# Kernel optimization log

Hardware: AMD Instinct MI355X
Metric: run time of the kernel (lower is better)

Reference implementation:

```python
import jax, jax.numpy as jnp
import numpy as np

H, DH = 16, 64          # num_heads, dim_head
DIM = 1024              # dim_ltn
EPS = 1e-5


def setup_inputs() -> dict:
    key = jax.random.key(0)
    ks = jax.random.split(key, 8)
    b, n_txt, t, m = 2, 2048, 4, 256
    text = jax.random.normal(ks[0], (b, n_txt, DIM), dtype=jnp.float32)
    image = jax.random.normal(ks[1], (b, t, m, DIM), dtype=jnp.float32)
    locations = jax.random.randint(ks[2], (b, n_txt), 0, 2)  # 0/1 media markers
    s = DIM ** -0.5
    Wq = jax.random.normal(ks[3], (DIM, H * DH), dtype=jnp.float32) * s
    Wkv = jax.random.normal(ks[4], (DIM, 2 * H * DH), dtype=jnp.float32) * s
    Wo = jax.random.normal(ks[5], (H * DH, DIM), dtype=jnp.float32) * s
    ln_gamma = jnp.ones((DIM,), dtype=jnp.float32)
    ln_beta = jnp.zeros((DIM,), dtype=jnp.float32)
    return {"text": text, "image": image, "locations": locations,
            "Wq": Wq, "Wkv": Wkv, "Wo": Wo,
            "ln_gamma": ln_gamma, "ln_beta": ln_beta}


def reference(text, image, locations, Wq, Wkv, Wo, ln_gamma, ln_beta):
    scale = DH ** -0.5
    b, t, m, d = image.shape
    # LayerNorm(text)
    mu = text.mean(-1, keepdims=True)
    var = ((text - mu) ** 2).mean(-1, keepdims=True)
    tn = (text - mu) / jnp.sqrt(var + EPS) * ln_gamma + ln_beta
    img = image.reshape(b, t * m, d)             # b (t m) d
    q = tn @ Wq                                  # b n (h dh)
    k, v = jnp.split(img @ Wkv, 2, axis=-1)      # each b tm (h dh)
    split_heads = lambda x: x.reshape(x.shape[0], x.shape[1], H, DH).transpose(0, 2, 1, 3)
    q, k, v = split_heads(q), split_heads(k), split_heads(v)
    attn = jnp.einsum('bhid,bhjd->bhij', q, k) * scale   # b h n (t m)
    txt_time = jnp.cumsum(locations, axis=-1)            # b n : media index per text token
    viz_time = jnp.repeat(jnp.arange(1, t + 1), m)       # (t m)
    # only_attend_to_immediate -> equality mask
    mask = txt_time[:, None, :, None] == viz_time[None, None, None, :]
    neg = -jnp.finfo(attn.dtype).max
    attn = jnp.where(mask, attn, neg)
    attn = jax.nn.softmax(attn, axis=-1)
    # zero attention for text tokens before any media (txt_time == 0)
    attn = jnp.where((txt_time == 0)[:, None, :, None], 0.0, attn)
    out = jnp.einsum('bhij,bhjd->bhid', attn, v)
    out = out.transpose(0, 2, 1, 3).reshape(b, -1, H * DH)
    return out @ Wo
```

## Files before the change

### kernel.cpp

```cpp
#include <hip/hip_runtime.h>

#define BATCH 2
#define NTXT  2048
#define TMED  4
#define MMED  256
#define TM    (TMED * MMED)
#define DIM   1024
#define NH    16
#define DHD   64
#define KVW   2048
#define RMAX  256
#define RT    32

typedef _Float16 f16x8 __attribute__((ext_vector_type(8)));
typedef float    f32x4 __attribute__((ext_vector_type(4)));

__global__ __launch_bounds__(1024) void k1_scan_cvt_tr(
    const int* __restrict__ loc, const float* __restrict__ image,
    const float* __restrict__ Wkv, int* __restrict__ tt, int* __restrict__ seg,
    float* __restrict__ ipart, _Float16* __restrict__ img16,
    _Float16* __restrict__ WkvT, float* __restrict__ zbase) {
  __shared__ float tile[64][65];
  __shared__ int wtot[16];
  __shared__ int wmin[2][16];
  const int idx = blockIdx.x;
  const int tid = threadIdx.x;
  if (idx < BATCH) {
    const int b = idx;
    const int lane = tid & 63, w = tid >> 6;
    const int e0 = tid * 2;
    const int a0 = loc[b * NTXT + e0], a1 = loc[b * NTXT + e0 + 1];
    const int p = a0 + a1;
    int incl = p;
#pragma unroll
    for (int off = 1; off < 64; off <<= 1) {
      const int t2 = __shfl_up(incl, off, 64);
      if (lane >= off) incl += t2;
    }
    if (lane == 63) wtot[w] = incl;
    __syncthreads();
    if (tid < 16) {
      const int v = wtot[tid];
      int inc2 = v;
#pragma unroll
      for (int off = 1; off < 16; off <<= 1) {
        const int t3 = __shfl_up(inc2, off, 64);
        if (tid >= off) inc2 += t3;
      }
      wtot[tid] = inc2 - v;
    }
    __syncthreads();
    const int base = wtot[w] + (incl - p);
    const int t0v = base + a0, t1v = t0v + a1;
    tt[b * NTXT + e0]     = t0v;
    tt[b * NTXT + e0 + 1] = t1v;
    {
      const int c1 = (t1v >= 1) ? ((t0v >= 1) ? e0 : e0 + 1) : NTXT;
      const int c5 = (t1v >= 5) ? ((t0v >= 5) ? e0 : e0 + 1) : NTXT;
      const unsigned long long b1 = __ballot(t1v >= 1);
      const unsigned long long b5 = __ballot(t1v >= 5);
      int m1 = NTXT, m5 = NTXT;
      if (b1) m1 = __shfl(c1, __ffsll(b1) - 1, 64);
      if (b5) m5 = __shfl(c5, __ffsll(b5) - 1, 64);
      if (lane == 0) { wmin[0][w] = m1; wmin[1][w] = m5; }
    }
    __syncthreads();
    if (tid == 0) {
      int s = NTXT, e = NTXT;
#pragma unroll
      for (int i = 0; i < 16; i++) {
        s = min(s, wmin[0][i]);
        e = min(e, wmin[1][i]);
      }
      seg[b * 2]     = s;
      seg[b * 2 + 1] = e - s;
    }
  } else if (idx < BATCH + 256) {
    const int j = idx - BATCH;
    const int b = j >> 7, rt = j & 127;
    const size_t base = (size_t)(b * TM + rt * 8) * DIM + tid;
    const float* p = image + base;
    _Float16* q = img16 + base;
    float s = 0.f;
#pragma unroll
    for (int r = 0; r < 8; r++) {
      const float v = p[(size_t)r * DIM];
      s += v;
      q[(size_t)r * DIM] = (_Float16)v;
    }
    ipart[(size_t)(b * 128 + rt) * DIM + tid] = s;
  } else if (idx < BATCH + 256 + 512) {
    const int j2 = idx - BATCH - 256;
    const int k0 = (j2 & 15) * 64, n0 = (j2 >> 4) * 64;
    const int r = tid >> 4, c4 = (tid & 15) * 4;
    const float4 v = *reinterpret_cast<const float4*>(
        Wkv + (size_t)(k0 + r) * KVW + n0 + c4);
    tile[r][c4 + 0] = v.x; tile[r][c4 + 1] = v.y;
    tile[r][c4 + 2] = v.z; tile[r][c4 + 3] = v.w;
    __syncthreads();
    if (tid < 512) {
      const int n = tid >> 3, kc = (tid & 7) * 8;
      f16x8 h;
#pragma unroll
      for (int u = 0; u < 8; u++) h[u] = (_Float16)tile[kc + u][n];
      *reinterpret_cast<f16x8*>(WkvT + (size_t)(n0 + n) * DIM + k0 + kc) = h;
    }
  } else {
    const int j = idx - (BATCH + 256 + 512);
    float4* z = reinterpret_cast<float4*>(zbase);
    const float4 zv = {0.f, 0.f, 0.f, 0.f};
    for (int i = j * 1024 + tid; i < 132096; i += 16 * 1024) z[i] = zv;
  }
}

__global__ __launch_bounds__(256) void k2_prep(
    const float* __restrict__ Wkv, const float* __restrict__ text,
    const float* __restrict__ gamma, const float* __restrict__ beta,
    const int* __restrict__ seg, const float* __restrict__ ipart,
    float* __restrict__ tn, float* __restrict__ vbar,
    float* __restrict__ out) {
  __shared__ float red[256];
  const int idx = blockIdx.x;
  const int tid = threadIdx.x;
  if (idx < 64) {
    const int b = idx >> 5, rt = idx & 31;
    const int i0 = seg[b * 2];
    const int cnt = min(seg[b * 2 + 1], RMAX);
    for (int r = rt; r < cnt; r += RT) {
      const float* xrow = text + (size_t)(b * NTXT + i0 + r) * DIM;
      float x[4];
      float s = 0.f;
#pragma unroll
      for (int u = 0; u < 4; u++) { x[u] = xrow[tid + 256 * u]; s += x[u]; }
      red[tid] = s; __syncthreads();
      for (int st = 128; st > 0; st >>= 1) {
        if (tid < st) red[tid] += red[tid + st];
        __syncthreads();
      }
      const float mu = red[0] * (1.0f / DIM); __syncthreads();
      float vs = 0.f;
#pragma unroll
      for (int u = 0; u < 4; u++) { float d = x[u] - mu; vs += d * d; }
      red[tid] = vs; __syncthreads();
      for (int st = 128; st > 0; st >>= 1) {
        if (tid < st) red[tid] += red[tid + st];
        __syncthreads();
      }
      const float rstd = rsqrtf(red[0] * (1.0f / DIM) + 1e-5f); __syncthreads();
      float* trow = tn + (size_t)(b * RMAX + r) * DIM;
#pragma unroll
      for (int u = 0; u < 4; u++) {
        const int c = tid + 256 * u;
        trow[c] = (x[u] - mu) * rstd * gamma[c] + beta[c];
      }
      __syncthreads();
    }
  } else if (idx < 128) {
    const int j = idx - 64;
    const int b = j >> 5, et = (j >> 3) & 3, cc = j & 7;
    const int e = et * 256 + tid;
    const int c0 = cc * 128;
    if (tid < 128) {
      float s = 0.f;
      for (int p = 0; p < 128; p++)
        s += ipart[(size_t)(b * 128 + p) * DIM + c0 + tid];
      red[tid] = s * (1.0f / (float)TM);
    }
    __syncthreads();
    float s = 0.f;
    for (int c = 0; c < 128; c++)
      s += red[c] * Wkv[(size_t)(c0 + c) * KVW + DIM + e];
    atomicAdd(&vbar[b * DIM + e], s);
  } else {
    const int b = idx - 128;
    const int i0 = seg[b * 2];
    const int cnt = min(seg[b * 2 + 1], RMAX);
    for (int r = 0; r < cnt; r++) {
      float* orow = out + (size_t)(b * NTXT + i0 + r) * DIM;
      for (int c = tid; c < DIM; c += 256) orow[c] = 0.f;
    }
  }
}

__global__ __launch_bounds__(512) void k3_gemm_qproj_obar(
    const _Float16* __restrict__ img16, const _Float16* __restrict__ WkvT,
    const float* __restrict__ Wq, const float* __restrict__ Wo,
    const float* __restrict__ tn, const float* __restrict__ vbar,
    const int* __restrict__ seg, _Float16* __restrict__ kv16,
    float* __restrict__ qbuf, float* __restrict__ obar) {
  __shared__ __align__(16) char smem[32768];
  const int idx = blockIdx.x;
  const int tid = threadIdx.x;
  if (idx < 256) {
    _Float16* As = (_Float16*)smem;
    _Float16* Bs = As + 128 * 64;
    const int lane = tid & 63, wid = tid >> 6;
    const int wm = wid & 3, wn = wid >> 2;
    const int row0 = (idx >> 4) * 128, col0 = (idx & 15) * 128;
    const int srow = tid >> 3, skc = (tid & 7) * 8;
    const int frow = lane & 15, fq = lane >> 4;
    const int swk = skc ^ ((srow & 7) << 3);
    f32x4 acc[2][4] = {};
    f16x8 a0v = *reinterpret_cast<const f16x8*>(
        img16 + (size_t)(row0 + srow) * DIM + skc);
    f16x8 a1v = *reinterpret_cast<const f16x8*>(
        img16 + (size_t)(row0 + srow + 64) * DIM + skc);
    f16x8 b0v = *reinterpret_cast<const f16x8*>(
        WkvT + (size_t)(col0 + srow) * DIM + skc);
    f16x8 b1v = *reinterpret_cast<const f16x8*>(
        WkvT + (size_t)(col0 + srow + 64) * DIM + skc);
    for (int k0 = 0; k0 < DIM; k0 += 64) {
      __syncthreads();
      *reinterpret_cast<f16x8*>(As + srow * 64 + swk)        = a0v;
      *reinterpret_cast<f16x8*>(As + (srow + 64) * 64 + swk) = a1v;
      *reinterpret_cast<f16x8*>(Bs + srow * 64 + swk)        = b0v;
      *reinterpret_cast<f16x8*>(Bs + (srow + 64) * 64 + swk) = b1v;
      __syncthreads();
      if (k0 + 64 < DIM) {
        a0v = *reinterpret_cast<const f16x8*>(
            img16 + (size_t)(row0 + srow) * DIM + k0 + 64 + skc);
        a1v = *reinterpret_cast<const f16x8*>(
            img16 + (size_t)(row0 + srow + 64) * DIM + k0 + 64 + skc);
        b0v = *reinterpret_cast<const f16x8*>(
            WkvT + (size_t)(col0 + srow) * DIM + k0 + 64 + skc);
        b1v = *reinterpret_cast<const f16x8*>(
            WkvT + (size_t)(col0 + srow + 64) * DIM + k0 + 64 + skc);
      }
      f16x8 af[2][2], bf[2][4];
#pragma unroll
      for (int kk = 0; kk < 2; kk++) {
#pragma unroll
        for (int mt = 0; mt < 2; mt++) {
          const int r = wm * 32 + mt * 16 + frow;
          af[kk][mt] = *reinterpret_cast<const f16x8*>(
              As + r * 64 + ((kk * 32 + fq * 8) ^ ((r & 7) << 3)));
        }
#pragma unroll
        for (int nt = 0; nt < 4; nt++) {
          const int c = wn * 64 + nt * 16 + frow;
          bf[kk][nt] = *reinterpret_cast<const f16x8*>(
              Bs + c * 64 + ((kk * 32 + fq * 8) ^ ((c & 7) << 3)));
        }
      }
#pragma unroll
      for (int kk = 0; kk < 2; kk++)
#pragma unroll
        for (int mt = 0; mt < 2; mt++)
#pragma unroll
          for (int nt = 0; nt < 4; nt++)
            acc[mt][nt] = __builtin_amdgcn_mfma_f32_16x16x32_f16(
                af[kk][mt], bf[kk][nt], acc[mt][nt], 0, 0, 0);
    }
#pragma unroll
    for (int mt = 0; mt < 2; mt++)
#pragma unroll
      for (int nt = 0; nt < 4; nt++) {
        const int col = col0 + wn * 64 + nt * 16 + frow;
#pragma unroll
        for (int r = 0; r < 4; r++) {
          const int row = row0 + wm * 32 + mt * 16 + fq * 4 + r;
          kv16[(size_t)row * KVW + col] = (_Float16)acc[mt][nt][r];
        }
      }
  } else if (idx < 320) {
    float* tn_s = (float*)smem;
    const int j = idx - 256;
    const int b = j >> 5, nt = (j >> 2) & 7, cc = j & 3;
    const int n0 = nt * 128, c0 = cc * 256;
    const int n = tid & 127, cs = tid >> 7;
    const int cnt = min(seg[b * 2 + 1], RMAX);
    for (int r0 = 0; r0 < cnt; r0 += 8) {
      const int rows = min(8, cnt - r0);
      for (int i = tid; i < 8 * 256; i += 512) {
        const int r = i >> 8, c = i & 255;
        tn_s[i] = (r < rows) ? tn[(size_t)(b * RMAX + r0 + r) * DIM + c0 + c]
                             : 0.f;
      }
      __syncthreads();
      float acc[8] = {};
      for (int ci = 0; ci < 64; ci++) {
        const int c = cs * 64 + ci;
        const float w = Wq[(size_t)(c0 + c) * DIM + n0 + n];
#pragma unroll
        for (int rr = 0; rr < 8; rr++) acc[rr] += tn_s[rr * 256 + c] * w;
      }
      for (int rr = 0; rr < rows; rr++)
        atomicAdd(&qbuf[(size_t)(b * RMAX + r0 + rr) * DIM + n0 + n], acc[rr]);
      __syncthreads();
    }
  } else {
    float* vb_s = (float*)smem;
    const int j = idx - 320;
    const int b = j >> 4, et = (j >> 3) & 1, cc = j & 7;
    const int e = et * 512 + tid;
    const int c0 = cc * 128;
    if (tid < 128) vb_s[tid] = vbar[b * DIM + c0 + tid];
    __syncthreads();
    float s = 0.f;
    for (int c = 0; c < 128; c++)
      s += vb_s[c] * Wo[(size_t)(c0 + c) * DIM + e];
    atomicAdd(&obar[b * DIM + e], s);
  }
}

__global__ __launch_bounds__(256) void k4_fill_attn(
    const float* __restrict__ text, const _Float16* __restrict__ kv16,
    const float* __restrict__ Wq, const float* __restrict__ Wo,
    const float* __restrict__ gamma, const float* __restrict__ beta,
    const int* __restrict__ tt, const int* __restrict__ seg,
    const float* __restrict__ obar, const float* __restrict__ qbuf,
    float* __restrict__ out) {
  __shared__ float red[256];
  __shared__ float pbuf[256];
  const int idx = blockIdx.x;
  const int tid = threadIdx.x;
  if (idx < BATCH * NTXT) {
    const int b = idx >> 11;
    const int i = idx & (NTXT - 1);
    const int t = tt[b * NTXT + i];
    float* orow = out + (size_t)(b * NTXT + i) * DIM;
    if (t == 0) {
      for (int c = tid; c < DIM; c += 256) orow[c] = 0.f;
      return;
    }
    if (t > TMED) {
      const float* ob = obar + b * DIM;
      for (int c = tid; c < DIM; c += 256) orow[c] = ob[c];
      return;
    }
    if (i - seg[b * 2] < RMAX) return;
    __shared__ float tns[DIM];
    __shared__ float qrow[DIM];
    __shared__ float oaccs[DIM];
    const float* xrow = text + (size_t)(b * NTXT + i) * DIM;
    float x[4];
    float s = 0.f;
#pragma unroll
    for (int u = 0; u < 4; u++) { x[u] = xrow[tid + 256 * u]; s += x[u]; }
    red[tid] = s; __syncthreads();
    for (int st = 128; st > 0; st >>= 1) {
      if (tid < st) red[tid] += red[tid + st];
      __syncthreads();
    }
    const float mu = red[0] * (1.0f / DIM); __syncthreads();
    float vs = 0.f;
#pragma unroll
    for (int u = 0; u < 4; u++) { float d = x[u] - mu; vs += d * d; }
    red[tid] = vs; __syncthreads();
    for (int st = 128; st > 0; st >>= 1) {
      if (tid < st) red[tid] += red[tid + st];
      __syncthreads();
    }
    const float rstd = rsqrtf(red[0] * (1.0f / DIM) + 1e-5f); __syncthreads();
#pragma unroll
    for (int u = 0; u < 4; u++) {
      const int c = tid + 256 * u;
      tns[c] = (x[u] - mu) * rstd * gamma[c] + beta[c];
    }
    __syncthreads();
    {
      float qa[4] = {0.f, 0.f, 0.f, 0.f};
      for (int c = 0; c < DIM; c++) {
        const float tv = tns[c];
        const float* w = Wq + (size_t)c * DIM + tid;
#pragma unroll
        for (int u = 0; u < 4; u++) qa[u] += tv * w[256 * u];
      }
#pragma unroll
      for (int u = 0; u < 4; u++) qrow[tid + 256 * u] = qa[u];
    }
    __syncthreads();
    const size_t kvrow0 = (size_t)(b * TM + (t - 1) * MMED) * KVW;
    const int d0 = tid & 63, g = tid >> 6;
    for (int h = 0; h < NH; h++) {
      const _Float16* krow = kv16 + kvrow0 + (size_t)tid * KVW + h * DHD;
      float sc = 0.f;
#pragma unroll
      for (int d = 0; d < DHD; d++) sc += qrow[h * DHD + d] * (float)krow[d];
      sc *= 0.125f;
      red[tid] = sc; __syncthreads();
      for (int st = 128; st > 0; st >>= 1) {
        if (tid < st) red[tid] = fmaxf(red[tid], red[tid + st]);
        __syncthreads();
      }
      const float mx = red[0]; __syncthreads();
      const float e = __expf(sc - mx);
      red[tid] = e; __syncthreads();
      for (int st = 128; st > 0; st >>= 1) {
        if (tid < st) red[tid] += red[tid + st];
        __syncthreads();
      }
      const float inv = 1.0f / red[0]; __syncthreads();
      pbuf[tid] = e * inv; __syncthreads();
      const _Float16* vbase = kv16 + kvrow0 + (size_t)(g * 64) * KVW + DIM + h * DHD + d0;
      float a = 0.f;
#pragma unroll 8
      for (int jj = 0; jj < 64; jj++) a += pbuf[g * 64 + jj] * (float)vbase[(size_t)jj * KVW];
      red[tid] = a; __syncthreads();
      if (tid < 64)
        oaccs[h * DHD + tid] = red[tid] + red[64 + tid] + red[128 + tid] + red[192 + tid];
      __syncthreads();
    }
    float oa[4] = {0.f, 0.f, 0.f, 0.f};
    for (int c = 0; c < DIM; c++) {
      const float ov = oaccs[c];
      const float* w = Wo + (size_t)c * DIM + tid;
#pragma unroll
      for (int u = 0; u < 4; u++) oa[u] += ov * w[256 * u];
    }
#pragma unroll
    for (int u = 0; u < 4; u++) orow[tid + 256 * u] = oa[u];
  } else {
    __shared__ float qs[DHD];
    __shared__ float osl[DHD];
    const int j = idx - BATCH * NTXT;
    const int h = j & 15, rt = (j >> 4) & 31, b = j >> 9;
    const int i0 = seg[b * 2];
    const int cnt = min(seg[b * 2 + 1], RMAX);
    const int d0 = tid & 63, g = tid >> 6;
    for (int r = rt; r < cnt; r += RT) {
      const int i = i0 + r;
      const int t = tt[b * NTXT + i];
      if (tid < 64) qs[tid] = qbuf[(size_t)(b * RMAX + r) * DIM + h * DHD + tid];
      __syncthreads();
      const size_t kvrow0 = (size_t)(b * TM + (t - 1) * MMED) * KVW;
      const _Float16* krow = kv16 + kvrow0 + (size_t)tid * KVW + h * DHD;
      float sc = 0.f;
#pragma unroll
      for (int d = 0; d < DHD; d += 8) {
        const f16x8 kk = *reinterpret_cast<const f16x8*>(krow + d);
#pragma unroll
        for (int u = 0; u < 8; u++) sc += qs[d + u] * (float)kk[u];
      }
      sc *= 0.125f;
      red[tid] = sc; __syncthreads();
      for (int st = 128; st > 0; st >>= 1) {
        if (tid < st) red[tid] = fmaxf(red[tid], red[tid + st]);
        __syncthreads();
      }
      const float mx = red[0]; __syncthreads();
      const float e = __expf(sc - mx);
      red[tid] = e; __syncthreads();
      for (int st = 128; st > 0; st >>= 1) {
        if (tid < st) red[tid] += red[tid + st];
        __syncthreads();
      }
      const float inv = 1.0f / red[0]; __syncthreads();
      pbuf[tid] = e * inv; __syncthreads();
      const _Float16* vbase = kv16 + kvrow0 + (size_t)(g * 64) * KVW + DIM + h * DHD + d0;
      float a = 0.f;
#pragma unroll 8
      for (int jj = 0; jj < 64; jj++) a += pbuf[g * 64 + jj] * (float)vbase[(size_t)jj * KVW];
      red[tid] = a; __syncthreads();
      if (tid < 64)
        osl[tid] = red[tid] + red[64 + tid] + red[128 + tid] + red[192 + tid];
      __syncthreads();
      float* orow = out + (size_t)(b * NTXT + i) * DIM;
#pragma unroll
      for (int u = 0; u < 4; u++) {
        const int c = tid + 256 * u;
        const float* w = Wo + (size_t)(h * DHD) * DIM + c;
        float s2 = 0.f;
#pragma unroll 8
        for (int d = 0; d < DHD; d++) s2 += osl[d] * w[(size_t)d * DIM];
        atomicAdd(&orow[c], s2);
      }
      __syncthreads();
    }
  }
}

extern "C" void kernel_launch(void* const* d_in, const int* in_sizes, int n_in,
                              void* d_out, int out_size, void* d_ws, size_t ws_size,
                              hipStream_t stream) {
  const float* text  = (const float*)d_in[0];
  const float* image = (const float*)d_in[1];
  const int*   loc   = (const int*)d_in[2];
  const float* Wq    = (const float*)d_in[3];
  const float* Wkv   = (const float*)d_in[4];
  const float* Wo    = (const float*)d_in[5];
  const float* gamma = (const float*)d_in[6];
  const float* beta  = (const float*)d_in[7];
  float* out = (float*)d_out;

  _Float16* kv16  = (_Float16*)d_ws;
  _Float16* WkvT  = kv16 + (size_t)BATCH * TM * KVW;
  _Float16* img16 = WkvT + (size_t)KVW * DIM;
  float*    tn    = (float*)(img16 + (size_t)BATCH * TM * DIM);
  float*    qbuf  = tn + (size_t)BATCH * RMAX * DIM;
  float*    vbar  = qbuf + (size_t)BATCH * RMAX * DIM;
  float*    obar  = vbar + BATCH * DIM;
  int*      tt    = (int*)(obar + BATCH * DIM);
  int*      seg   = tt + BATCH * NTXT;
  float*    ipart = (float*)(seg + 8);

  k1_scan_cvt_tr<<<BATCH + 256 + 512 + 16, 1024, 0, stream>>>(
      loc, image, Wkv, tt, seg, ipart, img16, WkvT, qbuf);
  k2_prep<<<130, 256, 0, stream>>>(Wkv, text, gamma, beta, seg, ipart,
                                   tn, vbar, out);
  k3_gemm_qproj_obar<<<352, 512, 0, stream>>>(img16, WkvT, Wq, Wo, tn, vbar,
                                              seg, kv16, qbuf, obar);
  k4_fill_attn<<<BATCH * NTXT + NH * RT * BATCH, 256, 0, stream>>>(
      text, kv16, Wq, Wo, gamma, beta, tt, seg, obar, qbuf, out);
}
```

Before: 152.8 us.

## Restructure attention by folding Wk into queries and Wv after probabilities

Replaces the full K/V projection GEMM over all image tokens with an algebraic reordering. Queries are multiplied by the per-head Wk slice to give U, scores are taken directly against fp16 image rows, and probabilities are multiplied by the transposed image before Wv and Wo are applied. This removes the large image×Wkv GEMM and the Wkv transpose. In exchange it adds six kernels with extra intermediate buffers (S, P16, pbar) and per-row scalar projection loops. Work now scales with the number of active rows times heads, so the cost depends on the media-marker layout.

```diff
diff --git a/kernel.cpp b/kernel.cpp
--- a/kernel.cpp
+++ b/kernel.cpp
@@ -10,463 +10,429 @@
 #define DHD   64
 #define KVW   2048
 #define RMAX  256
-#define RT    32
+#define MCAP  (RMAX * NH)
 
 typedef _Float16 f16x8 __attribute__((ext_vector_type(8)));
 typedef float    f32x4 __attribute__((ext_vector_type(4)));
 
-__global__ __launch_bounds__(1024) void k1_scan_cvt_tr(
+__device__ __forceinline__ void find5(const int* __restrict__ loc, int b,
+                                      int* posS, int tid) {
+  if (tid < 64) {
+    int pos[5] = {NTXT, NTXT, NTXT, NTXT, NTXT};
+    int found = 0;
+    for (int base = 0; base < NTXT && found < 5; base += 64) {
+      unsigned long long m = __ballot(loc[b * NTXT + base + tid] != 0);
+      while (m && found < 5) {
+        const int p = __ffsll(m) - 1;
+        pos[found++] = base + p;
+        m &= m - 1;
+      }
+    }
+    if (tid == 0) {
+#pragma unroll
+      for (int k = 0; k < 5; k++) posS[k] = pos[k];
+    }
+  }
+  __syncthreads();
+}
+
+__global__ __launch_bounds__(1024) void kA(
     const int* __restrict__ loc, const float* __restrict__ image,
-    const float* __restrict__ Wkv, int* __restrict__ tt, int* __restrict__ seg,
+    const float* __restrict__ text, const float* __restrict__ gamma,
+    const float* __restrict__ beta, int* __restrict__ seg,
     float* __restrict__ ipart, _Float16* __restrict__ img16,
-    _Float16* __restrict__ WkvT, float* __restrict__ zbase) {
-  __shared__ float tile[64][65];
-  __shared__ int wtot[16];
-  __shared__ int wmin[2][16];
+    _Float16* __restrict__ imgT16, float* __restrict__ tn,
+    float* __restrict__ out) {
+  __shared__ _Float16 cvt[32 * 1024];
+  __shared__ int posS[5];
+  __shared__ float wred[20];
   const int idx = blockIdx.x;
   const int tid = threadIdx.x;
   if (idx < BATCH) {
     const int b = idx;
-    const int lane = tid & 63, w = tid >> 6;
-    const int e0 = tid * 2;
-    const int a0 = loc[b * NTXT + e0], a1 = loc[b * NTXT + e0 + 1];
-    const int p = a0 + a1;
-    int incl = p;
-#pragma unroll
-    for (int off = 1; off < 64; off <<= 1) {
-      const int t2 = __shfl_up(incl, off, 64);
-      if (lane >= off) incl += t2;
-    }
-    if (lane == 63) wtot[w] = incl;
-    __syncthreads();
-    if (tid < 16) {
-      const int v = wtot[tid];
-      int inc2 = v;
-#pragma unroll
-      for (int off = 1; off < 16; off <<= 1) {
-        const int t3 = __shfl_up(inc2, off, 64);
-        if (tid >= off) inc2 += t3;
-      }
-      wtot[tid] = inc2 - v;
-    }
-    __syncthreads();
-    const int base = wtot[w] + (incl - p);
-    const int t0v = base + a0, t1v = t0v + a1;
-    tt[b * NTXT + e0]     = t0v;
-    tt[b * NTXT + e0 + 1] = t1v;
-    {
-      const int c1 = (t1v >= 1) ? ((t0v >= 1) ? e0 : e0 + 1) : NTXT;
-      const int c5 = (t1v >= 5) ? ((t0v >= 5) ? e0 : e0 + 1) : NTXT;
-      const unsigned long long b1 = __ballot(t1v >= 1);
-      const unsigned long long b5 = __ballot(t1v >= 5);
-      int m1 = NTXT, m5 = NTXT;
-      if (b1) m1 = __shfl(c1, __ffsll(b1) - 1, 64);
-      if (b5) m5 = __shfl(c5, __ffsll(b5) - 1, 64);
-      if (lane == 0) { wmin[0][w] = m1; wmin[1][w] = m5; }
-    }
-    __syncthreads();
+    find5(loc, b, posS, tid);
     if (tid == 0) {
-      int s = NTXT, e = NTXT;
-#pragma unroll
-      for (int i = 0; i < 16; i++) {
-        s = min(s, wmin[0][i]);
-        e = min(e, wmin[1][i]);
-      }
-      seg[b * 2]     = s;
-      seg[b * 2 + 1] = e - s;
-    }
-  } else if (idx < BATCH + 256) {
+#pragma unroll
+      for (int k = 0; k < 5; k++) seg[b * 8 + k] = posS[k];
+      int cnt = posS[4] - posS[0];
+      if (posS[0] >= NTXT) cnt = 0;
+      seg[b * 8 + 5] = min(cnt, RMAX);
+    }
+  } else if (idx < BATCH + 64) {
     const int j = idx - BATCH;
-    const int b = j >> 7, rt = j & 127;
-    const size_t base = (size_t)(b * TM + rt * 8) * DIM + tid;
-    const float* p = image + base;
-    _Float16* q = img16 + base;
+    const int b = j >> 5, jt = j & 31;
+    const int j0 = jt * 32;
+    const size_t rbase = (size_t)(b * TM + j0) * DIM + tid;
     float s = 0.f;
-#pragma unroll
-    for (int r = 0; r < 8; r++) {
-      const float v = p[(size_t)r * DIM];
+#pragma unroll 4
+    for (int r = 0; r < 32; r++) {
+      const float v = image[rbase + (size_t)r * DIM];
       s += v;
-      q[(size_t)r * DIM] = (_Float16)v;
-    }
-    ipart[(size_t)(b * 128 + rt) * DIM + tid] = s;
-  } else if (idx < BATCH + 256 + 512) {
-    const int j2 = idx - BATCH - 256;
-    const int k0 = (j2 & 15) * 64, n0 = (j2 >> 4) * 64;
-    const int r = tid >> 4, c4 = (tid & 15) * 4;
-    const float4 v = *reinterpret_cast<const float4*>(
-        Wkv + (size_t)(k0 + r) * KVW + n0 + c4);
-    tile[r][c4 + 0] = v.x; tile[r][c4 + 1] = v.y;
-    tile[r][c4 + 2] = v.z; tile[r][c4 + 3] = v.w;
-    __syncthreads();
-    if (tid < 512) {
-      const int n = tid >> 3, kc = (tid & 7) * 8;
-      f16x8 h;
-#pragma unroll
-      for (int u = 0; u < 8; u++) h[u] = (_Float16)tile[kc + u][n];
-      *reinterpret_cast<f16x8*>(WkvT + (size_t)(n0 + n) * DIM + k0 + kc) = h;
-    }
+      const _Float16 hv = (_Float16)v;
+      img16[rbase + (size_t)r * DIM] = hv;
+      cvt[r * 1024 + tid] = hv;
+    }
+    ipart[(b * 32 + jt) * 1024 + tid] = s;
+    __syncthreads();
+    f16x8 tv[4];
+#pragma unroll
+    for (int g = 0; g < 4; g++)
+#pragma unroll
+      for (int u = 0; u < 8; u++)
+        tv[g][u] = cvt[(g * 8 + u) * 1024 + tid];
+    _Float16* dst = imgT16 + (size_t)(b * DIM + tid) * TM + j0;
+#pragma unroll
+    for (int g = 0; g < 4; g++)
+      *reinterpret_cast<f16x8*>(dst + g * 8) = tv[g];
   } else {
-    const int j = idx - (BATCH + 256 + 512);
-    float4* z = reinterpret_cast<float4*>(zbase);
-    const float4 zv = {0.f, 0.f, 0.f, 0.f};
-    for (int i = j * 1024 + tid; i < 132096; i += 16 * 1024) z[i] = zv;
-  }
-}
-
-__global__ __launch_bounds__(256) void k2_prep(
-    const float* __restrict__ Wkv, const float* __restrict__ text,
-    const float* __restrict__ gamma, const float* __restrict__ beta,
-    const int* __restrict__ seg, const float* __restrict__ ipart,
-    float* __restrict__ tn, float* __restrict__ vbar,
-    float* __restrict__ out) {
-  __shared__ float red[256];
-  const int idx = blockIdx.x;
-  const int tid = threadIdx.x;
-  if (idx < 64) {
-    const int b = idx >> 5, rt = idx & 31;
-    const int i0 = seg[b * 2];
-    const int cnt = min(seg[b * 2 + 1], RMAX);
-    for (int r = rt; r < cnt; r += RT) {
-      const float* xrow = text + (size_t)(b * NTXT + i0 + r) * DIM;
-      float x[4];
-      float s = 0.f;
-#pragma unroll
-      for (int u = 0; u < 4; u++) { x[u] = xrow[tid + 256 * u]; s += x[u]; }
-      red[tid] = s; __syncthreads();
-      for (int st = 128; st > 0; st >>= 1) {
-        if (tid < st) red[tid] += red[tid + st];
+    const int b = idx - (BATCH + 64);
+    find5(loc, b, posS, tid);
+    const int pos0 = posS[0];
+    int cnt = posS[4] - pos0;
+    if (pos0 >= NTXT) cnt = 0;
+    cnt = min(cnt, RMAX);
+    for (int r = 0; r < cnt; r++) {
+      const float x = text[(size_t)(b * NTXT + pos0 + r) * DIM + tid];
+      float v = x;
+#pragma unroll
+      for (int off = 32; off; off >>= 1) v += __shfl_xor(v, off, 64);
+      if ((tid & 63) == 0) wred[tid >> 6] = v;
+      __syncthreads();
+      if (tid == 0) {
+        float t2 = 0.f;
+#pragma unroll
+        for (int q = 0; q < 16; q++) t2 += wred[q];
+        wred[16] = t2;
+      }
+      __syncthreads();
+      const float mu = wred[16] * (1.0f / DIM);
+      __syncthreads();
+      const float d = x - mu;
+      float v2 = d * d;
+#pragma unroll
+      for (int off = 32; off; off >>= 1) v2 += __shfl_xor(v2, off, 64);
+      if ((tid & 63) == 0) wred[tid >> 6] = v2;
+      __syncthreads();
+      if (tid == 0) {
+        float t2 = 0.f;
+#pragma unroll
+        for (int q = 0; q < 16; q++) t2 += wred[q];
+        wred[16] = t2;
+      }
+      __syncthreads();
+      const float rstd = rsqrtf(wred[16] * (1.0f / DIM) + 1e-5f);
+      __syncthreads();
+      tn[(size_t)(b * RMAX + r) * DIM + tid] = d * rstd * gamma[tid] + beta[tid];
+      out[(size_t)(b * NTXT + pos0 + r) * DIM + tid] = 0.f;
+    }
+  }
+}
+
+__global__ __launch_bounds__(256) void kB(
+    const float* __restrict__ Wq, const float* __restrict__ Wkv,
+    const float* __restrict__ tn, const int* __restrict__ seg,
+    const float* __restrict__ ipart, _Float16* __restrict__ U16,
+    float* __restrict__ vbar) {
+  __shared__ float tn_s[8 * 1024];
+  __shared__ float qred[4 * 8 * 64];
+  __shared__ float Qs[8 * 64];
+  __shared__ float wk_s[64 * 65];
+  __shared__ float ib_s[1024];
+  __shared__ float vred2[256];
+  const int idx = blockIdx.x;
+  const int tid = threadIdx.x;
+  if (idx < 32) {
+    const int b = idx >> 4, h = idx & 15;
+    const int cnt = seg[b * 8 + 5];
+    for (int ic0 = 0; ic0 < cnt; ic0 += 8) {
+      const int ni = min(8, cnt - ic0);
+      for (int k = tid; k < 8 * 1024; k += 256) {
+        const int r = k >> 10;
+        tn_s[k] = (r < ni) ? tn[(size_t)(b * RMAX + ic0 + r) * DIM + (k & 1023)]
+                           : 0.f;
+      }
+      __syncthreads();
+      {
+        const int d = tid & 63, cg = tid >> 6;
+        float qp[8] = {};
+        for (int c = cg * 256; c < cg * 256 + 256; c++) {
+          const float w = Wq[(size_t)c * DIM + h * DHD + d];
+#pragma unroll
+          for (int i2 = 0; i2 < 8; i2++) qp[i2] += tn_s[i2 * 1024 + c] * w;
+        }
+#pragma unroll
+        for (int i2 = 0; i2 < 8; i2++) qred[(cg * 8 + i2) * 64 + d] = qp[i2];
+      }
+      __syncthreads();
+      for (int k = tid; k < 512; k += 256) {
+        const int i2 = k >> 6, d = k & 63;
+        Qs[k] = qred[(0 * 8 + i2) * 64 + d] + qred[(1 * 8 + i2) * 64 + d] +
+                qred[(2 * 8 + i2) * 64 + d] + qred[(3 * 8 + i2) * 64 + d];
+      }
+      __syncthreads();
+      for (int cc = 0; cc < 16; cc++) {
+        for (int k = tid; k < 64 * 64; k += 256) {
+          const int row = k >> 6, col = k & 63;
+          wk_s[row * 65 + col] = Wkv[(size_t)(cc * 64 + row) * KVW + h * DHD + col];
+        }
         __syncthreads();
-      }
-      const float mu = red[0] * (1.0f / DIM); __syncthreads();
-      float vs = 0.f;
-#pragma unroll
-      for (int u = 0; u < 4; u++) { float d = x[u] - mu; vs += d * d; }
-      red[tid] = vs; __syncthreads();
-      for (int st = 128; st > 0; st >>= 1) {
-        if (tid < st) red[tid] += red[tid + st];
+        const int cl = tid & 63, ig = tid >> 6;
+#pragma unroll
+        for (int ii = 0; ii < 2; ii++) {
+          const int i2 = ig * 2 + ii;
+          if (i2 < ni) {
+            float u = 0.f;
+#pragma unroll 8
+            for (int d2 = 0; d2 < 64; d2++)
+              u += Qs[i2 * 64 + d2] * wk_s[cl * 65 + d2];
+            U16[((size_t)b * MCAP + (size_t)(ic0 + i2) * NH + h) * DIM +
+                cc * 64 + cl] = (_Float16)u;
+          }
+        }
         __syncthreads();
       }
-      const float rstd = rsqrtf(red[0] * (1.0f / DIM) + 1e-5f); __syncthreads();
-      float* trow = tn + (size_t)(b * RMAX + r) * DIM;
-#pragma unroll
-      for (int u = 0; u < 4; u++) {
-        const int c = tid + 256 * u;
-        trow[c] = (x[u] - mu) * rstd * gamma[c] + beta[c];
-      }
-      __syncthreads();
-    }
-  } else if (idx < 128) {
-    const int j = idx - 64;
-    const int b = j >> 5, et = (j >> 3) & 3, cc = j & 7;
-    const int e = et * 256 + tid;
-    const int c0 = cc * 128;
-    if (tid < 128) {
-      float s = 0.f;
-      for (int p = 0; p < 128; p++)
-        s += ipart[(size_t)(b * 128 + p) * DIM + c0 + tid];
-      red[tid] = s * (1.0f / (float)TM);
-    }
-    __syncthreads();
-    float s = 0.f;
-    for (int c = 0; c < 128; c++)
-      s += red[c] * Wkv[(size_t)(c0 + c) * KVW + DIM + e];
-    atomicAdd(&vbar[b * DIM + e], s);
+    }
   } else {
-    const int b = idx - 128;
-    const int i0 = seg[b * 2];
-    const int cnt = min(seg[b * 2 + 1], RMAX);
-    for (int r = 0; r < cnt; r++) {
-      float* orow = out + (size_t)(b * NTXT + i0 + r) * DIM;
-      for (int c = tid; c < DIM; c += 256) orow[c] = 0.f;
-    }
-  }
-}
-
-__global__ __launch_bounds__(512) void k3_gemm_qproj_obar(
-    const _Float16* __restrict__ img16, const _Float16* __restrict__ WkvT,
-    const float* __restrict__ Wq, const float* __restrict__ Wo,
-    const float* __restrict__ tn, const float* __restrict__ vbar,
-    const int* __restrict__ seg, _Float16* __restrict__ kv16,
-    float* __restrict__ qbuf, float* __restrict__ obar) {
+    const int j2 = idx - 32;
+    const int b = j2 >> 3, ec = j2 & 7;
+    for (int k = tid; k < 1024; k += 256) {
+      float s2 = 0.f;
+#pragma unroll 4
+      for (int p = 0; p < 32; p++) s2 += ipart[(b * 32 + p) * 1024 + k];
+      ib_s[k] = s2 * (1.0f / (float)TM);
+    }
+    __syncthreads();
+    const int e = ec * 128 + (tid & 127), half = tid >> 7;
+    float s2 = 0.f;
+    for (int c = half * 512; c < half * 512 + 512; c++)
+      s2 += ib_s[c] * Wkv[(size_t)c * KVW + DIM + e];
+    vred2[tid] = s2;
+    __syncthreads();
+    if (tid < 128)
+      vbar[b * DIM + ec * 128 + tid] = vred2[tid] + vred2[128 + tid];
+  }
+}
+
+__device__ __forceinline__ void gemm128_f32out(
+    const _Float16* __restrict__ Abase, const _Float16* __restrict__ Bbase,
+    float* __restrict__ Dbase, _Float16* As, _Float16* Bs, int tid) {
+  const int lane = tid & 63, wid = tid >> 6;
+  const int wm = wid & 3, wn = wid >> 2;
+  const int srow = tid >> 3, skc = (tid & 7) * 8;
+  const int frow = lane & 15, fq = lane >> 4;
+  const int swk = skc ^ ((srow & 7) << 3);
+  f32x4 acc[2][4] = {};
+  f16x8 a0v = *reinterpret_cast<const f16x8*>(Abase + (size_t)srow * 1024 + skc);
+  f16x8 a1v = *reinterpret_cast<const f16x8*>(Abase + (size_t)(srow + 64) * 1024 + skc);
+  f16x8 b0v = *reinterpret_cast<const f16x8*>(Bbase + (size_t)srow * 1024 + skc);
+  f16x8 b1v = *reinterpret_cast<const f16x8*>(Bbase + (size_t)(srow + 64) * 1024 + skc);
+  for (int k0 = 0; k0 < 1024; k0 += 64) {
+    __syncthreads();
+    *reinterpret_cast<f16x8*>(As + srow * 64 + swk) = a0v;
+    *reinterpret_cast<f16x8*>(As + (srow + 64) * 64 + swk) = a1v;
+    *reinterpret_cast<f16x8*>(Bs + srow * 64 + swk) = b0v;
+    *reinterpret_cast<f16x8*>(Bs + (srow + 64) * 64 + swk) = b1v;
+    __syncthreads();
+    if (k0 + 64 < 1024) {
+      a0v = *reinterpret_cast<const f16x8*>(Abase + (size_t)srow * 1024 + k0 + 64 + skc);
+      a1v = *reinterpret_cast<const f16x8*>(Abase + (size_t)(srow + 64) * 1024 + k0 + 64 + skc);
+      b0v = *reinterpret_cast<const f16x8*>(Bbase + (size_t)srow * 1024 + k0 + 64 + skc);
+      b1v = *reinterpret_cast<const f16x8*>(Bbase + (size_t)(srow + 64) * 1024 + k0 + 64 + skc);
+    }
+    f16x8 af[2][2], bf[2][4];
+#pragma unroll
+    for (int kk = 0; kk < 2; kk++) {
+#pragma unroll
+      for (int mt = 0; mt < 2; mt++) {
+        const int r = wm * 32 + mt * 16 + frow;
+        af[kk][mt] = *reinterpret_cast<const f16x8*>(
+            As + r * 64 + ((kk * 32 + fq * 8) ^ ((r & 7) << 3)));
+      }
+#pragma unroll
+      for (int nt = 0; nt < 4; nt++) {
+        const int c = wn * 64 + nt * 16 + frow;
+        bf[kk][nt] = *reinterpret_cast<const f16x8*>(
+            Bs + c * 64 + ((kk * 32 + fq * 8) ^ ((c & 7) << 3)));
+      }
+    }
+#pragma unroll
+    for (int kk = 0; kk < 2; kk++)
+#pragma unroll
+      for (int mt = 0; mt < 2; mt++)
+#pragma unroll
+        for (int nt = 0; nt < 4; nt++)
+          acc[mt][nt] = __builtin_amdgcn_mfma_f32_16x16x32_f16(
+              af[kk][mt], bf[kk][nt], acc[mt][nt], 0, 0, 0);
+  }
+#pragma unroll
+  for (int mt = 0; mt < 2; mt++)
+#pragma unroll
+    for (int nt = 0; nt < 4; nt++) {
+      const int col = wn * 64 + nt * 16 + frow;
+#pragma unroll
+      for (int r = 0; r < 4; r++) {
+        const int row = wm * 32 + mt * 16 + fq * 4 + r;
+        Dbase[(size_t)row * 1024 + col] = acc[mt][nt][r];
+      }
+    }
+}
+
+__global__ __launch_bounds__(512) void kC(
+    const _Float16* __restrict__ U16, const _Float16* __restrict__ img16,
+    const float* __restrict__ vbar, const float* __restrict__ Wo,
+    const int* __restrict__ seg, float* __restrict__ S,
+    float* __restrict__ obar) {
   __shared__ __align__(16) char smem[32768];
-  const int idx = blockIdx.x;
-  const int tid = threadIdx.x;
-  if (idx < 256) {
+  __shared__ float vb_s[1024];
+  __shared__ float ored[512];
+  const int idx = blockIdx.x;
+  const int tid = threadIdx.x;
+  if (idx < 512) {
+    const int b = idx >> 8;
+    const int li = idx & 255;
+    const int mt = li >> 3, nt = li & 7;
+    const int cnt16 = seg[b * 8 + 5] * NH;
+    const int row0 = mt * 128;
+    if (row0 >= cnt16) return;
+    const int col0 = nt * 128;
     _Float16* As = (_Float16*)smem;
     _Float16* Bs = As + 128 * 64;
-    const int lane = tid & 63, wid = tid >> 6;
-    const int wm = wid & 3, wn = wid >> 2;
-    const int row0 = (idx >> 4) * 128, col0 = (idx & 15) * 128;
-    const int srow = tid >> 3, skc = (tid & 7) * 8;
-    const int frow = lane & 15, fq = lane >> 4;
-    const int swk = skc ^ ((srow & 7) << 3);
-    f32x4 acc[2][4] = {};
-    f16x8 a0v = *reinterpret_cast<const f16x8*>(
-        img16 + (size_t)(row0 + srow) * DIM + skc);
-    f16x8 a1v = *reinterpret_cast<const f16x8*>(
-        img16 + (size_t)(row0 + srow + 64) * DIM + skc);
-    f16x8 b0v = *reinterpret_cast<const f16x8*>(
-        WkvT + (size_t)(col0 + srow) * DIM + skc);
-    f16x8 b1v = *reinterpret_cast<const f16x8*>(
-        WkvT + (size_t)(col0 + srow + 64) * DIM + skc);
-    for (int k0 = 0; k0 < DIM; k0 += 64) {
-      __syncthreads();
-      *reinterpret_cast<f16x8*>(As + srow * 64 + swk)        = a0v;
-      *reinterpret_cast<f16x8*>(As + (srow + 64) * 64 + swk) = a1v;
-      *reinterpret_cast<f16x8*>(Bs + srow * 64 + swk)        = b0v;
-      *reinterpret_cast<f16x8*>(Bs + (srow + 64) * 64 + swk) = b1v;
-      __syncthreads();
-      if (k0 + 64 < DIM) {
-        a0v = *reinterpret_cast<const f16x8*>(
-            img16 + (size_t)(row0 + srow) * DIM + k0 + 64 + skc);
-        a1v = *reinterpret_cast<const f16x8*>(
-            img16 + (size_t)(row0 + srow + 64) * DIM + k0 + 64 + skc);
-        b0v = *reinterpret_cast<const f16x8*>(
-            WkvT + (size_t)(col0 + srow) * DIM + k0 + 64 + skc);
-        b1v = *reinterpret_cast<const f16x8*>(
-            WkvT + (size_t)(col0 + srow + 64) * DIM + k0 + 64 + skc);
-      }
-      f16x8 af[2][2], bf[2][4];
-#pragma unroll
-      for (int kk = 0; kk < 2; kk++) {
-#pragma unroll
-        for (int mt = 0; mt < 2; mt++) {
-          const int r = wm * 32 + mt * 16 + frow;
-          af[kk][mt] = *reinterpret_cast<const f16x8*>(
-              As + r * 64 + ((kk * 32 + fq * 8) ^ ((r & 7) << 3)));
-        }
-#pragma unroll
-        for (int nt = 0; nt < 4; nt++) {
-          const int c = wn * 64 + nt * 16 + frow;
-          bf[kk][nt] = *reinterpret_cast<const f16x8*>(
-              Bs + c * 64 + ((kk * 32 + fq * 8) ^ ((c & 7) << 3)));
-        }
-      }
-#pragma unroll
-      for (int kk = 0; kk < 2; kk++)
-#pragma unroll
-        for (int mt = 0; mt < 2; mt++)
-#pragma unroll
-          for (int nt = 0; nt < 4; nt++)
-            acc[mt][nt] = __builtin_amdgcn_mfma_f32_16x16x32_f16(
-                af[kk][mt], bf[kk][nt], acc[mt][nt], 0, 0, 0);
-    }
-#pragma unroll
-    for (int mt = 0; mt < 2; mt++)
-#pragma unroll
-      for (int nt = 0; nt < 4; nt++) {
-        const int col = col0 + wn * 64 + nt * 16 + frow;
-#pragma unroll
-        for (int r = 0; r < 4; r++) {
-          const int row = row0 + wm * 32 + mt * 16 + fq * 4 + r;
-          kv16[(size_t)row * KVW + col] = (_Float16)acc[mt][nt][r];
-        }
-      }
-  } else if (idx < 320) {
-    float* tn_s = (float*)smem;
-    const int j = idx - 256;
-    const int b = j >> 5, nt = (j >> 2) & 7, cc = j & 3;
-    const int n0 = nt * 128, c0 = cc * 256;
-    const int n = tid & 127, cs = tid >> 7;
-    const int cnt = min(seg[b * 2 + 1], RMAX);
-    for (int r0 = 0; r0 < cnt; r0 += 8) {
-      const int rows = min(8, cnt - r0);
-      for (int i = tid; i < 8 * 256; i += 512) {
-        const int r = i >> 8, c = i & 255;
-        tn_s[i] = (r < rows) ? tn[(size_t)(b * RMAX + r0 + r) * DIM + c0 + c]
-                             : 0.f;
-      }
-      __syncthreads();
-      float acc[8] = {};
-      for (int ci = 0; ci < 64; ci++) {
-        const int c = cs * 64 + ci;
-        const float w = Wq[(size_t)(c0 + c) * DIM + n0 + n];
-#pragma unroll
-        for (int rr = 0; rr < 8; rr++) acc[rr] += tn_s[rr * 256 + c] * w;
-      }
-      for (int rr = 0; rr < rows; rr++)
-        atomicAdd(&qbuf[(size_t)(b * RMAX + r0 + rr) * DIM + n0 + n], acc[rr]);
-      __syncthreads();
-    }
+    gemm128_f32out(U16 + ((size_t)b * MCAP + row0) * DIM,
+                   img16 + ((size_t)b * TM + col0) * DIM,
+                   S + ((size_t)b * MCAP + row0) * TM + col0, As, Bs, tid);
   } else {
-    float* vb_s = (float*)smem;
-    const int j = idx - 320;
-    const int b = j >> 4, et = (j >> 3) & 1, cc = j & 7;
-    const int e = et * 512 + tid;
-    const int c0 = cc * 128;
-    if (tid < 128) vb_s[tid] = vbar[b * DIM + c0 + tid];
-    __syncthreads();
-    float s = 0.f;
-    for (int c = 0; c < 128; c++)
-      s += vb_s[c] * Wo[(size_t)(c0 + c) * DIM + e];
-    atomicAdd(&obar[b * DIM + e], s);
-  }
-}
-
-__global__ __launch_bounds__(256) void k4_fill_attn(
-    const float* __restrict__ text, const _Float16* __restrict__ kv16,
-    const float* __restrict__ Wq, const float* __restrict__ Wo,
-    const float* __restrict__ gamma, const float* __restrict__ beta,
-    const int* __restrict__ tt, const int* __restrict__ seg,
-    const float* __restrict__ obar, const float* __restrict__ qbuf,
+    const int j2 = idx - 512;
+    const int b = j2 >> 3, ec = j2 & 7;
+    for (int k = tid; k < 1024; k += 512) vb_s[k] = vbar[b * DIM + k];
+    __syncthreads();
+    const int e = ec * 128 + (tid & 127), qg = tid >> 7;
+    float s2 = 0.f;
+    for (int c = qg * 256; c < qg * 256 + 256; c++)
+      s2 += vb_s[c] * Wo[(size_t)c * DIM + e];
+    ored[tid] = s2;
+    __syncthreads();
+    if (tid < 128)
+      obar[b * DIM + ec * 128 + tid] =
+          ored[tid] + ored[128 + tid] + ored[256 + tid] + ored[384 + tid];
+  }
+}
+
+__global__ __launch_bounds__(256) void kD(
+    const float* __restrict__ S, const int* __restrict__ seg,
+    const float* __restrict__ obar, _Float16* __restrict__ P16,
     float* __restrict__ out) {
-  __shared__ float red[256];
-  __shared__ float pbuf[256];
+  __shared__ float wred[4];
   const int idx = blockIdx.x;
   const int tid = threadIdx.x;
   if (idx < BATCH * NTXT) {
     const int b = idx >> 11;
     const int i = idx & (NTXT - 1);
-    const int t = tt[b * NTXT + i];
+    const int pos0 = seg[b * 8 + 0];
+    const int pos4 = seg[b * 8 + 4];
     float* orow = out + (size_t)(b * NTXT + i) * DIM;
-    if (t == 0) {
-      for (int c = tid; c < DIM; c += 256) orow[c] = 0.f;
-      return;
-    }
-    if (t > TMED) {
+    if (i < pos0) {
+#pragma unroll
+      for (int u = 0; u < 4; u++) orow[tid + 256 * u] = 0.f;
+    } else if (i >= pos4) {
       const float* ob = obar + b * DIM;
-      for (int c = tid; c < DIM; c += 256) orow[c] = ob[c];
-      return;
-    }
-    if (i - seg[b * 2] < RMAX) return;
-    __shared__ float tns[DIM];
-    __shared__ float qrow[DIM];
-    __shared__ float oaccs[DIM];
-    const float* xrow = text + (size_t)(b * NTXT + i) * DIM;
-    float x[4];
-    float s = 0.f;
-#pragma unroll
-    for (int u = 0; u < 4; u++) { x[u] = xrow[tid + 256 * u]; s += x[u]; }
-    red[tid] = s; __syncthreads();
-    for (int st = 128; st > 0; st >>= 1) {
-      if (tid < st) red[tid] += red[tid + st];
-      __syncthreads();
-    }
-    const float mu = red[0] * (1.0f / DIM); __syncthreads();
-    float vs = 0.f;
-#pragma unroll
-    for (int u = 0; u < 4; u++) { float d = x[u] - mu; vs += d * d; }
-    red[tid] = vs; __syncthreads();
-    for (int st = 128; st > 0; st >>= 1) {
-      if (tid < st) red[tid] += red[tid + st];
-      __syncthreads();
-    }
-    const float rstd = rsqrtf(red[0] * (1.0f / DIM) + 1e-5f); __syncthreads();
+#pragma unroll
+      for (int u = 0; u < 4; u++) orow[tid + 256 * u] = ob[tid + 256 * u];
+    }
+  } else {
+    const int j2 = idx - BATCH * NTXT;
+    const int b = j2 >> 8, i = j2 & 255;
+    const int cnt = seg[b * 8 + 5];
+    if (i >= cnt) return;
+    const int pos0 = seg[b * 8 + 0];
+    const int ig = pos0 + i;
+    const int t = 1 + (ig >= seg[b * 8 + 1]) + (ig >= seg[b * 8 + 2]) +
+                  (ig >= seg[b * 8 + 3]);
+    const int joff = (t - 1) * MMED;
+    const int lane = tid & 63, w = tid >> 6;
+    for (int h = 0; h < NH; h++) {
+      const int m = i * NH + h;
+      const float v = S[((size_t)b * MCAP + m) * TM + joff + tid] * 0.125f;
+      float mv = v;
+#pragma unroll
+      for (int off = 32; off; off >>= 1) mv = fmaxf(mv, __shfl_xor(mv, off, 64));
+      if (lane == 0) wred[w] = mv;
+      __syncthreads();
+      mv = fmaxf(fmaxf(wred[0], wred[1]), fmaxf(wred[2], wred[3]));
+      const float e = __expf(v - mv);
+      float sv = e;
+#pragma unroll
+      for (int off = 32; off; off >>= 1) sv += __shfl_xor(sv, off, 64);
+      __syncthreads();
+      if (lane == 0) wred[w] = sv;
+      __syncthreads();
+      sv = wred[0] + wred[1] + wred[2] + wred[3];
+      const float p = e / sv;
+      _Float16* prow = P16 + ((size_t)b * MCAP + m) * TM;
+#pragma unroll
+      for (int u = 0; u < 4; u++)
+        prow[tid + 256 * u] = (u == t - 1) ? (_Float16)p : (_Float16)0.f;
+      __syncthreads();
+    }
+  }
+}
+
+__global__ __launch_bounds__(512) void kE(
+    const _Float16* __restrict__ P16, const _Float16* __restrict__ imgT16,
+    const int* __restrict__ seg, float* __restrict__ pbar) {
+  __shared__ __align__(16) char smem[32768];
+  const int idx = blockIdx.x;
+  const int tid = threadIdx.x;
+  const int b = idx >> 8;
+  const int li = idx & 255;
+  const int mt = li >> 3, nt = li & 7;
+  const int cnt16 = seg[b * 8 + 5] * NH;
+  const int row0 = mt * 128;
+  if (row0 >= cnt16) return;
+  const int col0 = nt * 128;
+  _Float16* As = (_Float16*)smem;
+  _Float16* Bs = As + 128 * 64;
+  gemm128_f32out(P16 + ((size_t)b * MCAP + row0) * TM,
+                 imgT16 + ((size_t)b * DIM + col0) * TM,
+                 pbar + ((size_t)b * MCAP + row0) * DIM + col0, As, Bs, tid);
+}
+
+__global__ __launch_bounds__(256) void kF(
+    const float* __restrict__ pbar, const float* __restrict__ Wkv,
+    const float* __restrict__ Wo, const int* __restrict__ seg,
+    float* __restrict__ out) {
+  __shared__ float pb_s[1024];
+  __shared__ float ared[256];
+  __shared__ float av_s[64];
+  const int idx = blockIdx.x;
+  const int tid = threadIdx.x;
+  const int b = idx >> 6, h = (idx >> 2) & 15, ic = idx & 3;
+  const int pos0 = seg[b * 8 + 0];
+  const int cnt = seg[b * 8 + 5];
+  for (int i = ic; i < cnt; i += 4) {
+    const int m = i * NH + h;
+    for (int k = tid; k < 1024; k += 256)
+      pb_s[k] = pbar[((size_t)b * MCAP + m) * DIM + k];
+    __syncthreads();
+    const int d = tid & 63, cg = tid >> 6;
+    float a = 0.f;
+    for (int c = cg * 256; c < cg * 256 + 256; c++)
+      a += pb_s[c] * Wkv[(size_t)c * KVW + DIM + h * DHD + d];
+    ared[cg * 64 + d] = a;
+    __syncthreads();
+    if (tid < 64)
+      av_s[tid] = ared[tid] + ared[64 + tid] + ared[128 + tid] + ared[192 + tid];
+    __syncthreads();
+    float* orow = out + (size_t)(b * NTXT + pos0 + i) * DIM;
 #pragma unroll
     for (int u = 0; u < 4; u++) {
-      const int c = tid + 256 * u;
-      tns[c] = (x[u] - mu) * rstd * gamma[c] + beta[c];
-    }
-    __syncthreads();
-    {
-      float qa[4] = {0.f, 0.f, 0.f, 0.f};
-      for (int c = 0; c < DIM; c++) {
-        const float tv = tns[c];
-        const float* w = Wq + (size_t)c * DIM + tid;
-#pragma unroll
-        for (int u = 0; u < 4; u++) qa[u] += tv * w[256 * u];
-      }
-#pragma unroll
-      for (int u = 0; u < 4; u++) qrow[tid + 256 * u] = qa[u];
-    }
-    __syncthreads();
-    const size_t kvrow0 = (size_t)(b * TM + (t - 1) * MMED) * KVW;
-    const int d0 = tid & 63, g = tid >> 6;
-    for (int h = 0; h < NH; h++) {
-      const _Float16* krow = kv16 + kvrow0 + (size_t)tid * KVW + h * DHD;
-      float sc = 0.f;
-#pragma unroll
-      for (int d = 0; d < DHD; d++) sc += qrow[h * DHD + d] * (float)krow[d];
-      sc *= 0.125f;
-      red[tid] = sc; __syncthreads();
-      for (int st = 128; st > 0; st >>= 1) {
-        if (tid < st) red[tid] = fmaxf(red[tid], red[tid + st]);
-        __syncthreads();
-      }
-      const float mx = red[0]; __syncthreads();
-      const float e = __expf(sc - mx);
-      red[tid] = e; __syncthreads();
-      for (int st = 128; st > 0; st >>= 1) {
-        if (tid < st) red[tid] += red[tid + st];
-        __syncthreads();
-      }
-      const float inv = 1.0f / red[0]; __syncthreads();
-      pbuf[tid] = e * inv; __syncthreads();
-      const _Float16* vbase = kv16 + kvrow0 + (size_t)(g * 64) * KVW + DIM + h * DHD + d0;
-      float a = 0.f;
+      const int e = tid + 256 * u;
+      float o = 0.f;
 #pragma unroll 8
-      for (int jj = 0; jj < 64; jj++) a += pbuf[g * 64 + jj] * (float)vbase[(size_t)jj * KVW];
-      red[tid] = a; __syncthreads();
-      if (tid < 64)
-        oaccs[h * DHD + tid] = red[tid] + red[64 + tid] + red[128 + tid] + red[192 + tid];
-      __syncthreads();
-    }
-    float oa[4] = {0.f, 0.f, 0.f, 0.f};
-    for (int c = 0; c < DIM; c++) {
-      const float ov = oaccs[c];
-      const float* w = Wo + (size_t)c * DIM + tid;
-#pragma unroll
-      for (int u = 0; u < 4; u++) oa[u] += ov * w[256 * u];
-    }
-#pragma unroll
-    for (int u = 0; u < 4; u++) orow[tid + 256 * u] = oa[u];
-  } else {
-    __shared__ float qs[DHD];
-    __shared__ float osl[DHD];
-    const int j = idx - BATCH * NTXT;
-    const int h = j & 15, rt = (j >> 4) & 31, b = j >> 9;
-    const int i0 = seg[b * 2];
-    const int cnt = min(seg[b * 2 + 1], RMAX);
-    const int d0 = tid & 63, g = tid >> 6;
-    for (int r = rt; r < cnt; r += RT) {
-      const int i = i0 + r;
-      const int t = tt[b * NTXT + i];
-      if (tid < 64) qs[tid] = qbuf[(size_t)(b * RMAX + r) * DIM + h * DHD + tid];
-      __syncthreads();
-      const size_t kvrow0 = (size_t)(b * TM + (t - 1) * MMED) * KVW;
-      const _Float16* krow = kv16 + kvrow0 + (size_t)tid * KVW + h * DHD;
-      float sc = 0.f;
-#pragma unroll
-      for (int d = 0; d < DHD; d += 8) {
-        const f16x8 kk = *reinterpret_cast<const f16x8*>(krow + d);
-#pragma unroll
-        for (int u = 0; u < 8; u++) sc += qs[d + u] * (float)kk[u];
-      }
-      sc *= 0.125f;
-      red[tid] = sc; __syncthreads();
-      for (int st = 128; st > 0; st >>= 1) {
-        if (tid < st) red[tid] = fmaxf(red[tid], red[tid + st]);
-        __syncthreads();
-      }
-      const float mx = red[0]; __syncthreads();
-      const float e = __expf(sc - mx);
-      red[tid] = e; __syncthreads();
-      for (int st = 128; st > 0; st >>= 1) {
-        if (tid < st) red[tid] += red[tid + st];
-        __syncthreads();
-      }
-      const float inv = 1.0f / red[0]; __syncthreads();
-      pbuf[tid] = e * inv; __syncthreads();
-      const _Float16* vbase = kv16 + kvrow0 + (size_t)(g * 64) * KVW + DIM + h * DHD + d0;
-      float a = 0.f;
-#pragma unroll 8
-      for (int jj = 0; jj < 64; jj++) a += pbuf[g * 64 + jj] * (float)vbase[(size_t)jj * KVW];
-      red[tid] = a; __syncthreads();
-      if (tid < 64)
-        osl[tid] = red[tid] + red[64 + tid] + red[128 + tid] + red[192 + tid];
-      __syncthreads();
-      float* orow = out + (size_t)(b * NTXT + i) * DIM;
-#pragma unroll
-      for (int u = 0; u < 4; u++) {
-        const int c = tid + 256 * u;
-        const float* w = Wo + (size_t)(h * DHD) * DIM + c;
-        float s2 = 0.f;
-#pragma unroll 8
-        for (int d = 0; d < DHD; d++) s2 += osl[d] * w[(size_t)d * DIM];
-        atomicAdd(&orow[c], s2);
-      }
-      __syncthreads();
-    }
+      for (int d2 = 0; d2 < 64; d2++)
+        o += av_s[d2] * Wo[(size_t)(h * DHD + d2) * DIM + e];
+      atomicAdd(&orow[e], o);
+    }
+    __syncthreads();
   }
 }
 
@@ -483,23 +449,23 @@
   const float* beta  = (const float*)d_in[7];
   float* out = (float*)d_out;
 
-  _Float16* kv16  = (_Float16*)d_ws;
-  _Float16* WkvT  = kv16 + (size_t)BATCH * TM * KVW;
-  _Float16* img16 = WkvT + (size_t)KVW * DIM;
-  float*    tn    = (float*)(img16 + (size_t)BATCH * TM * DIM);
-  float*    qbuf  = tn + (size_t)BATCH * RMAX * DIM;
-  float*    vbar  = qbuf + (size_t)BATCH * RMAX * DIM;
-  float*    obar  = vbar + BATCH * DIM;
-  int*      tt    = (int*)(obar + BATCH * DIM);
-  int*      seg   = tt + BATCH * NTXT;
-  float*    ipart = (float*)(seg + 8);
-
-  k1_scan_cvt_tr<<<BATCH + 256 + 512 + 16, 1024, 0, stream>>>(
-      loc, image, Wkv, tt, seg, ipart, img16, WkvT, qbuf);
-  k2_prep<<<130, 256, 0, stream>>>(Wkv, text, gamma, beta, seg, ipart,
-                                   tn, vbar, out);
-  k3_gemm_qproj_obar<<<352, 512, 0, stream>>>(img16, WkvT, Wq, Wo, tn, vbar,
-                                              seg, kv16, qbuf, obar);
-  k4_fill_attn<<<BATCH * NTXT + NH * RT * BATCH, 256, 0, stream>>>(
-      text, kv16, Wq, Wo, gamma, beta, tt, seg, obar, qbuf, out);
-}
+  _Float16* img16  = (_Float16*)d_ws;
+  _Float16* imgT16 = img16 + (size_t)BATCH * TM * DIM;
+  _Float16* U16    = imgT16 + (size_t)BATCH * DIM * TM;
+  _Float16* P16    = U16 + (size_t)BATCH * MCAP * DIM;
+  float*    S      = (float*)(P16 + (size_t)BATCH * MCAP * TM);
+  float*    pbar   = S + (size_t)BATCH * MCAP * TM;
+  float*    tn     = pbar + (size_t)BATCH * MCAP * DIM;
+  float*    ipart  = tn + (size_t)BATCH * RMAX * DIM;
+  float*    vbar   = ipart + BATCH * 32 * DIM;
+  float*    obar   = vbar + BATCH * DIM;
+  int*      seg    = (int*)(obar + BATCH * DIM);
+
+  kA<<<BATCH + 64 + BATCH, 1024, 0, stream>>>(loc, image, text, gamma, beta,
+                                              seg, ipart, img16, imgT16, tn, out);
+  kB<<<48, 256, 0, stream>>>(Wq, Wkv, tn, seg, ipart, U16, vbar);
+  kC<<<528, 512, 0, stream>>>(U16, img16, vbar, Wo, seg, S, obar);
+  kD<<<BATCH * NTXT + 512, 256, 0, stream>>>(S, seg, obar, P16, out);
+  kE<<<512, 512, 0, stream>>>(P16, imgT16, seg, pbar);
+  kF<<<128, 256, 0, stream>>>(pbar, Wkv, Wo, seg, out);
+}
```

Result: slower. 498.3 us (+226.1%).
